# Performance work log

Measured on AMD Instinct MI355X. Metric: run time of the kernel, lower is better.

The kernel has to match this reference:

```python
import jax, jax.numpy as jnp
import numpy as np


def setup_inputs() -> dict:
    key = jax.random.key(0)
    k1, k2 = jax.random.split(key)
    B, D, K = 8192, 4096, 16
    x = jax.random.normal(k1, (B, D), dtype=jnp.float32)
    # kaiming_uniform_(a=sqrt(5)) on [K, D]: bound = sqrt(6/((1+5)*fan_in)) = 1/sqrt(D)
    bound = 1.0 / np.sqrt(D)
    w = jax.random.uniform(k2, (K, D), dtype=jnp.float32, minval=-bound, maxval=bound)
    return {"x": x, "w": w}


def reference(x, w):
    # z[b,d] = x[b,d] * (1 + sum_{i=1..k} w[i-1,d] * x[b,(d+i) mod D])
    k = w.shape[0]
    acc = jnp.ones_like(x)
    for i in range(1, k + 1):
        acc = acc + w[i - 1][None, :] * jnp.roll(x, -i, axis=1)
    return x * acc
```

## Files before the change

kernel.cpp:

```cpp
#include <hip/hip_runtime.h>


#define D 4096
#define DG 1024
#define K 16
#define TPB 256
#define RPB 16

typedef float f32x4 __attribute__((ext_vector_type(4)));

__global__ __launch_bounds__(TPB) void quad_enhancer_kernel(
    const float* __restrict__ x, const float* __restrict__ w,
    float* __restrict__ out) {
  const int tid = threadIdx.x;
  const int cg = blockIdx.x * TPB + tid;
  const int b0 = blockIdx.y * RPB;

  const float4* __restrict__ x4 = (const float4*)x;
  const float4* __restrict__ w4 = (const float4*)w;
  f32x4* __restrict__ out4 = (f32x4*)out;

  const int g1 = (cg + 1) & (DG - 1);
  const int g2 = (cg + 2) & (DG - 1);
  const int g3 = (cg + 3) & (DG - 1);
  const int g4 = (cg + 4) & (DG - 1);

  float4 wv[K];
#pragma unroll
  for (int i = 0; i < K; ++i) wv[i] = w4[i * DG + cg];

  auto loadrow = [&](int b, float4* buf) {
    const float4* __restrict__ xr = x4 + (size_t)b * DG;
    buf[0] = xr[cg];
    buf[1] = xr[g1];
    buf[2] = xr[g2];
    buf[3] = xr[g3];
    buf[4] = xr[g4];
  };

  auto compute_store = [&](int b, const float4* buf) {
    float xs[20];
#pragma unroll
    for (int j = 0; j < 5; ++j) {
      xs[4 * j + 0] = buf[j].x;
      xs[4 * j + 1] = buf[j].y;
      xs[4 * j + 2] = buf[j].z;
      xs[4 * j + 3] = buf[j].w;
    }
    float ax = 1.0f, ay = 1.0f, az = 1.0f, aw = 1.0f;
#pragma unroll
    for (int i = 0; i < K; ++i) {
      ax = fmaf(wv[i].x, xs[i + 1], ax);
      ay = fmaf(wv[i].y, xs[i + 2], ay);
      az = fmaf(wv[i].z, xs[i + 3], az);
      aw = fmaf(wv[i].w, xs[i + 4], aw);
    }
    f32x4 o;
    o.x = xs[0] * ax;
    o.y = xs[1] * ay;
    o.z = xs[2] * az;
    o.w = xs[3] * aw;
    __builtin_nontemporal_store(o, &out4[(size_t)b * DG + cg]);
  };

  float4 bufA[5], bufB[5];
  loadrow(b0, bufA);
#pragma unroll 1
  for (int r = 0; r < RPB; r += 2) {
    loadrow(b0 + r + 1, bufB);
    compute_store(b0 + r, bufA);
    if (r + 2 < RPB) loadrow(b0 + r + 2, bufA);
    compute_store(b0 + r + 1, bufB);
  }
}

extern "C" void kernel_launch(void* const* d_in, const int* in_sizes, int n_in,
                              void* d_out, int out_size, void* d_ws, size_t ws_size,
                              hipStream_t stream) {
  const float* x = (const float*)d_in[0];
  const float* w = (const float*)d_in[1];
  float* out = (float*)d_out;
  const int B = in_sizes[0] / D;

  dim3 grid(DG / TPB, B / RPB);
  quad_enhancer_kernel<<<grid, TPB, 0, stream>>>(x, w, out);
}
```

Baseline: 256.4 us.

## Map one row-chunk per thread and reload weights instead of register-caching them

Replaces the per-block 16-row double-buffered loop with a flat grid where each thread handles one float4 of one row. Weights are no longer held in registers across rows but loaded from cache per output, cutting register pressure and raising occupancy and parallelism. The trade-off is extra weight load traffic (16 float4 loads per output) through L1/L2 and loss of the explicit software prefetch.

```diff
diff --git a/kernel.cpp b/kernel.cpp
--- a/kernel.cpp
+++ b/kernel.cpp
@@ -5,73 +5,48 @@
 #define DG 1024
 #define K 16
 #define TPB 256
-#define RPB 16
 
 typedef float f32x4 __attribute__((ext_vector_type(4)));
 
 __global__ __launch_bounds__(TPB) void quad_enhancer_kernel(
     const float* __restrict__ x, const float* __restrict__ w,
     float* __restrict__ out) {
-  const int tid = threadIdx.x;
-  const int cg = blockIdx.x * TPB + tid;
-  const int b0 = blockIdx.y * RPB;
+  const int gid = blockIdx.x * TPB + threadIdx.x;
+  const int cg = gid & (DG - 1);
+  const int b = gid >> 10;
 
-  const float4* __restrict__ x4 = (const float4*)x;
+  const float4* __restrict__ xr = (const float4*)x + (size_t)b * DG;
   const float4* __restrict__ w4 = (const float4*)w;
-  f32x4* __restrict__ out4 = (f32x4*)out;
 
-  const int g1 = (cg + 1) & (DG - 1);
-  const int g2 = (cg + 2) & (DG - 1);
-  const int g3 = (cg + 3) & (DG - 1);
-  const int g4 = (cg + 4) & (DG - 1);
+  float4 v0 = xr[cg];
+  float4 v1 = xr[(cg + 1) & (DG - 1)];
+  float4 v2 = xr[(cg + 2) & (DG - 1)];
+  float4 v3 = xr[(cg + 3) & (DG - 1)];
+  float4 v4 = xr[(cg + 4) & (DG - 1)];
 
-  float4 wv[K];
+  float xs[20];
+  xs[0] = v0.x; xs[1] = v0.y; xs[2] = v0.z; xs[3] = v0.w;
+  xs[4] = v1.x; xs[5] = v1.y; xs[6] = v1.z; xs[7] = v1.w;
+  xs[8] = v2.x; xs[9] = v2.y; xs[10] = v2.z; xs[11] = v2.w;
+  xs[12] = v3.x; xs[13] = v3.y; xs[14] = v3.z; xs[15] = v3.w;
+  xs[16] = v4.x; xs[17] = v4.y; xs[18] = v4.z; xs[19] = v4.w;
+
+  float ax = 1.0f, ay = 1.0f, az = 1.0f, aw = 1.0f;
 #pragma unroll
-  for (int i = 0; i < K; ++i) wv[i] = w4[i * DG + cg];
+  for (int i = 0; i < K; ++i) {
+    float4 wv = w4[i * DG + cg];
+    ax = fmaf(wv.x, xs[i + 1], ax);
+    ay = fmaf(wv.y, xs[i + 2], ay);
+    az = fmaf(wv.z, xs[i + 3], az);
+    aw = fmaf(wv.w, xs[i + 4], aw);
+  }
 
-  auto loadrow = [&](int b, float4* buf) {
-    const float4* __restrict__ xr = x4 + (size_t)b * DG;
-    buf[0] = xr[cg];
-    buf[1] = xr[g1];
-    buf[2] = xr[g2];
-    buf[3] = xr[g3];
-    buf[4] = xr[g4];
-  };
-
-  auto compute_store = [&](int b, const float4* buf) {
-    float xs[20];
-#pragma unroll
-    for (int j = 0; j < 5; ++j) {
-      xs[4 * j + 0] = buf[j].x;
-      xs[4 * j + 1] = buf[j].y;
-      xs[4 * j + 2] = buf[j].z;
-      xs[4 * j + 3] = buf[j].w;
-    }
-    float ax = 1.0f, ay = 1.0f, az = 1.0f, aw = 1.0f;
-#pragma unroll
-    for (int i = 0; i < K; ++i) {
-      ax = fmaf(wv[i].x, xs[i + 1], ax);
-      ay = fmaf(wv[i].y, xs[i + 2], ay);
-      az = fmaf(wv[i].z, xs[i + 3], az);
-      aw = fmaf(wv[i].w, xs[i + 4], aw);
-    }
-    f32x4 o;
-    o.x = xs[0] * ax;
-    o.y = xs[1] * ay;
-    o.z = xs[2] * az;
-    o.w = xs[3] * aw;
-    __builtin_nontemporal_store(o, &out4[(size_t)b * DG + cg]);
-  };
-
-  float4 bufA[5], bufB[5];
-  loadrow(b0, bufA);
-#pragma unroll 1
-  for (int r = 0; r < RPB; r += 2) {
-    loadrow(b0 + r + 1, bufB);
-    compute_store(b0 + r, bufA);
-    if (r + 2 < RPB) loadrow(b0 + r + 2, bufA);
-    compute_store(b0 + r + 1, bufB);
-  }
+  f32x4 o;
+  o.x = xs[0] * ax;
+  o.y = xs[1] * ay;
+  o.z = xs[2] * az;
+  o.w = xs[3] * aw;
+  __builtin_nontemporal_store(o, (f32x4*)out + (size_t)b * DG + cg);
 }
 
 extern "C" void kernel_launch(void* const* d_in, const int* in_sizes, int n_in,
@@ -82,6 +57,6 @@
   float* out = (float*)d_out;
   const int B = in_sizes[0] / D;
 
-  dim3 grid(DG / TPB, B / RPB);
-  quad_enhancer_kernel<<<grid, TPB, 0, stream>>>(x, w, out);
+  const int nblocks = (B * DG) / TPB;
+  quad_enhancer_kernel<<<dim3(nblocks), dim3(TPB), 0, stream>>>(x, w, out);
 }
```

New measurement: 338.1 us. 1.32x slower.
